# Kernel tuning notes

Hardware: AMD Instinct MI355X
Metric: run time of the kernel (lower is better)

The kernel has to match this reference:

```python
import jax, jax.numpy as jnp
import numpy as np

T, B, I, H, L, O = 512, 64, 128, 512, 2, 256


def _lstm_layer(x, Wih, Whh, b):
    """One LSTM layer over time. x:[T,B,in] -> (ys:[T,B,H], hT:[B,H], cT:[B,H]).
    PyTorch gate order: i, f, g, o. Zero initial state (module's zero buffers)."""
    Hs = Whh.shape[1]
    # Precompute input contribution for all timesteps (one big GEMM).
    xg = jnp.einsum('tbi,gi->tbg', x, Wih) + b  # [T,B,4H]

    def step(carry, xt):
        h, c = carry
        g = xt + h @ Whh.T  # [B,4H]
        i, f, gg, o = jnp.split(g, 4, axis=-1)
        c = jax.nn.sigmoid(f) * c + jax.nn.sigmoid(i) * jnp.tanh(gg)
        h = jax.nn.sigmoid(o) * jnp.tanh(c)
        return (h, c), h

    h0 = jnp.zeros((x.shape[1], Hs), x.dtype)
    (hT, cT), ys = jax.lax.scan(step, (h0, h0), xg)
    return ys, hT, cT


def setup_inputs() -> dict:
    key = jax.random.key(0)
    ks = jax.random.split(key, 9)
    s = 1.0 / np.sqrt(H)  # torch default uniform(-1/sqrt(H), 1/sqrt(H)) scale
    u = lambda k, shp: jax.random.uniform(k, shp, jnp.float32, -s, s)
    return {
        'x': jax.random.normal(ks[0], (T, B, I), jnp.float32),
        'W_ih0': u(ks[1], (4 * H, I)),
        'W_hh0': u(ks[2], (4 * H, H)),
        'b0': u(ks[3], (4 * H,)),  # b_ih + b_hh combined
        'W_ih1': u(ks[4], (4 * H, H)),
        'W_hh1': u(ks[5], (4 * H, H)),
        'b1': u(ks[6], (4 * H,)),
        'fc_w': u(ks[7], (O, H)),
        'fc_b': u(ks[8], (O,)),
    }


def reference(x, W_ih0, W_hh0, b0, W_ih1, W_hh1, b1, fc_w, fc_b):
    y0, h0, c0 = _lstm_layer(x, W_ih0, W_hh0, b0)
    y1, h1, c1 = _lstm_layer(y0, W_ih1, W_hh1, b1)
    fc = jnp.einsum('tbh,oh->tbo', y1, fc_w) + fc_b  # fused output projection
    hN = jnp.stack([h0, h1])  # [L,B,H]
    cN = jnp.stack([c0, c1])
    return fc, (hN, cN)
```

## Files before the change

kernel.cpp:

```cpp
#include <hip/hip_runtime.h>
#include <hip/hip_bf16.h>

#define T_SEQ 512
#define BATCH 64
#define IN0   128
#define HID   512
#define OUTF  256
#define G4    (4*HID)
#define NWG_L 64
#define FSTR  32

typedef __attribute__((ext_vector_type(8))) short short8;
typedef __attribute__((ext_vector_type(4))) float f32x4;
typedef unsigned short u16;
typedef unsigned long long u64;

__device__ __forceinline__ float sigmoidf_(float x) { return 1.f / (1.f + __expf(-x)); }
__device__ __forceinline__ float tanhf_(float x)    { return 1.f - 2.f / (1.f + __expf(2.f * x)); }

__device__ __forceinline__ u16 f2bf(float f) {
    union { float f; unsigned u; } a; a.f = f;
    unsigned u = a.u;
    return (u16)((u + 0x7fffu + ((u >> 16) & 1u)) >> 16);
}

__device__ __forceinline__ void poll_grp(const unsigned* flags, int lane, int grp, unsigned tgt) {
    const unsigned* p = flags + (size_t)(grp * 16 + (lane & 15)) * FSTR;
    unsigned it = 0;
    for (;;) {
        unsigned v = __hip_atomic_load(p, __ATOMIC_RELAXED, __HIP_MEMORY_SCOPE_AGENT);
        if (__all((int)(v >= tgt))) return;
        if (it < 6) __builtin_amdgcn_s_sleep(1);
        else        __builtin_amdgcn_s_sleep(16);
        if ((++it & 1023u) == 0u)
            (void)__hip_atomic_load(p, __ATOMIC_ACQUIRE, __HIP_MEMORY_SCOPE_AGENT);
    }
}

__global__ void cvt_f32_bf16(const float* __restrict__ in, u16* __restrict__ out, int n4) {
    int i = blockIdx.x * blockDim.x + threadIdx.x;
    if (i < n4) {
        float4 v = reinterpret_cast<const float4*>(in)[i];
        ushort4 o;
        o.x = f2bf(v.x); o.y = f2bf(v.y); o.z = f2bf(v.z); o.w = f2bf(v.w);
        reinterpret_cast<ushort4*>(out)[i] = o;
    }
}

template<int LAYER>
__device__ __forceinline__ void run_layer(
    const u16* __restrict__ asrc,
    const u16* __restrict__ wih, const u16* __restrict__ whh,
    const float* __restrict__ bias,
    u16* __restrict__ ybuf,
    float* __restrict__ hNout, float* __restrict__ cNout,
    unsigned* flags_own, unsigned* flags_dep, int g,
    u16 (*lds_w)[32][512], float (*lds_g)[33], float (*lds_b)[16],
    unsigned (*lds_h)[4])
{
    constexpr int KIN = (LAYER == 0) ? IN0 : HID;
    constexpr int KS1 = KIN / 32;
    constexpr int KS  = KS1 + 16;

    const int tid  = threadIdx.x;
    const int lane = tid & 63;
    const int w    = tid >> 6;
    const int ubase = 8 * g;

    for (int idx = tid; idx < 2 * KS * 64; idx += 256) {
        int nt  = (idx >= KS * 64) ? 1 : 0;
        int rem = idx - nt * KS * 64;
        int ks = rem >> 6, s = rem & 63, q = s & 15, kq = s >> 4;
        int r = (q >> 2) * HID + ubase + 4 * nt + (q & 3);
        const u16* src = (ks < KS1)
            ? wih + (size_t)r * KIN + (size_t)ks * 32 + kq * 8
            : whh + (size_t)r * HID + (size_t)(ks - KS1) * 32 + kq * 8;
        *reinterpret_cast<uint4*>(&lds_w[nt][ks][s * 8]) =
            *reinterpret_cast<const uint4*>(src);
    }
    if (tid < 32) {
        int nt = tid >> 4, q = tid & 15;
        lds_b[nt][q] = bias[(q >> 2) * HID + ubase + 4 * nt + (q & 3)];
    }
    __syncthreads();

    const int pb  = tid & 63;
    const int pu2 = tid >> 6;
    float c0 = 0.f, c1 = 0.f;

    const int arow = 16 * w + (lane & 15);
    const int koff = (lane >> 4) * 8;

    for (int t = 0; t < T_SEQ; ++t) {
        f32x4 ac0[4] = {{0,0,0,0},{0,0,0,0},{0,0,0,0},{0,0,0,0}};
        f32x4 ac1[4] = {{0,0,0,0},{0,0,0,0},{0,0,0,0},{0,0,0,0}};

        if (LAYER == 0) {
            const u16* ap = asrc + ((size_t)t * BATCH + arow) * KIN + koff;
            short8 a[KS1];
            #pragma unroll
            for (int j = 0; j < KS1; ++j)
                a[j] = *reinterpret_cast<const short8*>(ap + j * 32);
            #pragma unroll
            for (int j = 0; j < KS1; ++j) {
                ac0[j & 3] = __builtin_amdgcn_mfma_f32_16x16x32_bf16(
                    a[j], *reinterpret_cast<const short8*>(&lds_w[0][j][lane * 8]), ac0[j & 3], 0, 0, 0);
                ac1[j & 3] = __builtin_amdgcn_mfma_f32_16x16x32_bf16(
                    a[j], *reinterpret_cast<const short8*>(&lds_w[1][j][lane * 8]), ac1[j & 3], 0, 0, 0);
            }
        } else {
            const u16* ap = asrc + ((size_t)t * BATCH + arow) * HID + koff;
            for (int grp = 0; grp < 4; ++grp) {
                poll_grp(flags_dep, lane, grp, (unsigned)(t + 1));
                #pragma unroll
                for (int j = 0; j < 4; ++j) {
                    int ks = grp * 4 + j;
                    short8 a = *reinterpret_cast<const short8*>(ap + ks * 32);
                    ac0[j] = __builtin_amdgcn_mfma_f32_16x16x32_bf16(
                        a, *reinterpret_cast<const short8*>(&lds_w[0][ks][lane * 8]), ac0[j], 0, 0, 0);
                    ac1[j] = __builtin_amdgcn_mfma_f32_16x16x32_bf16(
                        a, *reinterpret_cast<const short8*>(&lds_w[1][ks][lane * 8]), ac1[j], 0, 0, 0);
                }
            }
        }

        if (t > 0) {
            const u16* hp = ybuf + ((size_t)(t - 1) * BATCH + arow) * HID + koff;
            for (int grp = 0; grp < 4; ++grp) {
                poll_grp(flags_own, lane, grp, (unsigned)t);
                #pragma unroll
                for (int j = 0; j < 4; ++j) {
                    int ks = grp * 4 + j;
                    short8 a = *reinterpret_cast<const short8*>(hp + ks * 32);
                    ac0[j] = __builtin_amdgcn_mfma_f32_16x16x32_bf16(
                        a, *reinterpret_cast<const short8*>(&lds_w[0][KS1 + ks][lane * 8]), ac0[j], 0, 0, 0);
                    ac1[j] = __builtin_amdgcn_mfma_f32_16x16x32_bf16(
                        a, *reinterpret_cast<const short8*>(&lds_w[1][KS1 + ks][lane * 8]), ac1[j], 0, 0, 0);
                }
            }
        }

        f32x4 s0 = (ac0[0] + ac0[1]) + (ac0[2] + ac0[3]);
        f32x4 s1 = (ac1[0] + ac1[1]) + (ac1[2] + ac1[3]);
        #pragma unroll
        for (int j = 0; j < 4; ++j) {
            int row = 16 * w + (lane >> 4) * 4 + j;
            lds_g[row][lane & 15]        = s0[j];
            lds_g[row][16 + (lane & 15)] = s1[j];
        }
        __syncthreads();

        {
            const int nt = pu2 >> 1;
            const int dq = (2 * pu2) & 3;
            const float* gr = &lds_g[pb][nt * 16];
            const float* br = lds_b[nt];
            float gi0 = sigmoidf_(gr[dq]      + br[dq]);
            float gf0 = sigmoidf_(gr[4 + dq]  + br[4 + dq]);
            float gg0 = tanhf_(   gr[8 + dq]  + br[8 + dq]);
            float go0 = sigmoidf_(gr[12 + dq] + br[12 + dq]);
            c0 = gf0 * c0 + gi0 * gg0;
            float h0v = go0 * tanhf_(c0);
            float gi1 = sigmoidf_(gr[dq + 1]      + br[dq + 1]);
            float gf1 = sigmoidf_(gr[4 + dq + 1]  + br[4 + dq + 1]);
            float gg1 = tanhf_(   gr[8 + dq + 1]  + br[8 + dq + 1]);
            float go1 = sigmoidf_(gr[12 + dq + 1] + br[12 + dq + 1]);
            c1 = gf1 * c1 + gi1 * gg1;
            float h1v = go1 * tanhf_(c1);

            lds_h[pb][pu2] = (unsigned)f2bf(h0v) | ((unsigned)f2bf(h1v) << 16);

            if (t == T_SEQ - 1) {
                const int u0 = ubase + 4 * nt + dq, u1 = u0 + 1;
                hNout[pb * HID + u0] = h0v;
                hNout[pb * HID + u1] = h1v;
                cNout[pb * HID + u0] = c0;
                cNout[pb * HID + u1] = c1;
            }
        }
        __syncthreads();

        if (w == 0) {
            uint4 hv = *reinterpret_cast<const uint4*>(&lds_h[lane][0]);
            u64 q0 = (u64)hv.x | ((u64)hv.y << 32);
            u64 q1 = (u64)hv.z | ((u64)hv.w << 32);
            u64* yp = reinterpret_cast<u64*>(
                ybuf + ((size_t)t * BATCH + lane) * HID + ubase);
            __hip_atomic_store(yp + 0, q0, __ATOMIC_RELAXED, __HIP_MEMORY_SCOPE_AGENT);
            __hip_atomic_store(yp + 1, q1, __ATOMIC_RELAXED, __HIP_MEMORY_SCOPE_AGENT);
            asm volatile("s_waitcnt vmcnt(0)" ::: "memory");
            if (lane == 0)
                __hip_atomic_store(flags_own + (size_t)g * FSTR, (unsigned)(t + 1),
                                   __ATOMIC_RELAXED, __HIP_MEMORY_SCOPE_AGENT);
        }
    }
}

__global__ __launch_bounds__(256, 1)
void lstm_fused(const u16* __restrict__ x_bf,
                const u16* __restrict__ wih0, const u16* __restrict__ whh0, const float* __restrict__ b0,
                const u16* __restrict__ wih1, const u16* __restrict__ whh1, const float* __restrict__ b1,
                u16* __restrict__ y0, u16* __restrict__ y1,
                float* __restrict__ hN, float* __restrict__ cN,
                unsigned* __restrict__ ctr)
{
    __shared__ __align__(16) u16 lds_w[2][32][512];
    __shared__ float lds_g[BATCH][33];
    __shared__ float lds_b[2][16];
    __shared__ __align__(16) unsigned lds_h[BATCH][4];

    unsigned* flags0 = ctr;
    unsigned* flags1 = ctr + NWG_L * FSTR;

    const int wgid = blockIdx.x;
    if (wgid < NWG_L) {
        run_layer<0>(x_bf, wih0, whh0, b0, y0, hN, cN,
                     flags0, flags0, wgid, lds_w, lds_g, lds_b, lds_h);
    } else {
        run_layer<1>(y0, wih1, whh1, b1, y1, hN + BATCH * HID, cN + BATCH * HID,
                     flags1, flags0, wgid - NWG_L, lds_w, lds_g, lds_b, lds_h);
    }
}

__global__ __launch_bounds__(256)
void fc_kernel(const u16* __restrict__ y1, const u16* __restrict__ fcw,
               const float* __restrict__ fcb, float* __restrict__ out)
{
    const int tid  = threadIdx.x;
    const int lane = tid & 63;
    const int wgid = blockIdx.x * 4 + (tid >> 6);
    const int nq   = wgid & 3;
    const int mt0  = wgid >> 2;

    for (int j = 0; j < 8; ++j) {
        int mt = mt0 + j * 256;
        f32x4 acc[4] = {{0,0,0,0},{0,0,0,0},{0,0,0,0},{0,0,0,0}};
        const u16* arow = y1 + ((size_t)mt * 16 + (lane & 15)) * HID + (lane >> 4) * 8;
        #pragma unroll
        for (int ks = 0; ks < 16; ++ks) {
            short8 a = *reinterpret_cast<const short8*>(arow + ks * 32);
            #pragma unroll
            for (int nt = 0; nt < 4; ++nt) {
                const u16* brow = fcw + ((size_t)(nq * 64 + nt * 16 + (lane & 15))) * HID
                                      + ks * 32 + (lane >> 4) * 8;
                short8 b = *reinterpret_cast<const short8*>(brow);
                acc[nt] = __builtin_amdgcn_mfma_f32_16x16x32_bf16(a, b, acc[nt], 0, 0, 0);
            }
        }
        #pragma unroll
        for (int nt = 0; nt < 4; ++nt) {
            int col = nq * 64 + nt * 16 + (lane & 15);
            float bb = fcb[col];
            #pragma unroll
            for (int jj = 0; jj < 4; ++jj) {
                int row = mt * 16 + (lane >> 4) * 4 + jj;
                out[(size_t)row * OUTF + col] = acc[nt][jj] + bb;
            }
        }
    }
}

extern "C" void kernel_launch(void* const* d_in, const int* in_sizes, int n_in,
                              void* d_out, int out_size, void* d_ws, size_t ws_size,
                              hipStream_t stream)
{
    const float* x    = (const float*)d_in[0];
    const float* wih0 = (const float*)d_in[1];
    const float* whh0 = (const float*)d_in[2];
    const float* b0   = (const float*)d_in[3];
    const float* wih1 = (const float*)d_in[4];
    const float* whh1 = (const float*)d_in[5];
    const float* b1   = (const float*)d_in[6];
    const float* fcw  = (const float*)d_in[7];
    const float* fcb  = (const float*)d_in[8];
    float* out = (float*)d_out;

    const size_t flag_bytes = (size_t)2 * NWG_L * FSTR * 4;

    char* ws = (char*)d_ws;
    size_t off = 0;
    unsigned* ctr = (unsigned*)ws;                    off += flag_bytes;
    u16* x_bf    = (u16*)(ws + off);                  off += (size_t)T_SEQ * BATCH * IN0 * 2;
    u16* wih0_bf = (u16*)(ws + off);                  off += (size_t)G4 * IN0 * 2;
    u16* whh0_bf = (u16*)(ws + off);                  off += (size_t)G4 * HID * 2;
    u16* wih1_bf = (u16*)(ws + off);                  off += (size_t)G4 * HID * 2;
    u16* whh1_bf = (u16*)(ws + off);                  off += (size_t)G4 * HID * 2;
    u16* fcw_bf  = (u16*)(ws + off);                  off += (size_t)OUTF * HID * 2;
    u16* y0      = (u16*)(ws + off);                  off += (size_t)T_SEQ * BATCH * HID * 2;
    u16* y1      = (u16*)(ws + off);                  off += (size_t)T_SEQ * BATCH * HID * 2;

    hipMemsetAsync(ctr, 0, flag_bytes, stream);

    auto conv = [&](const float* in, u16* o, int n) {
        int n4 = n / 4;
        cvt_f32_bf16<<<(n4 + 255) / 256, 256, 0, stream>>>(in, o, n4);
    };
    conv(x,    x_bf,    T_SEQ * BATCH * IN0);
    conv(wih0, wih0_bf, G4 * IN0);
    conv(whh0, whh0_bf, G4 * HID);
    conv(wih1, wih1_bf, G4 * HID);
    conv(whh1, whh1_bf, G4 * HID);
    conv(fcw,  fcw_bf,  OUTF * HID);

    float* outFC = out;
    float* hN = out + (size_t)T_SEQ * BATCH * OUTF;
    float* cN = hN + 2 * BATCH * HID;

    lstm_fused<<<2 * NWG_L, 256, 0, stream>>>(x_bf, wih0_bf, whh0_bf, b0,
                                              wih1_bf, whh1_bf, b1,
                                              y0, y1, hN, cN, ctr);
    fc_kernel<<<256, 256, 0, stream>>>(y1, fcw_bf, fcb, outFC);
}
```

Measured before the change: 3.302 ms.

## Halve LSTM workgroups per layer, each owning 16 hidden units

```diff
diff --git a/kernel.cpp b/kernel.cpp
--- a/kernel.cpp
+++ b/kernel.cpp
@@ -7,7 +7,7 @@
 #define HID   512
 #define OUTF  256
 #define G4    (4*HID)
-#define NWG_L 64
+#define NWG_L 32
 #define FSTR  32
 
 typedef __attribute__((ext_vector_type(8))) short short8;
@@ -25,7 +25,7 @@
 }
 
 __device__ __forceinline__ void poll_grp(const unsigned* flags, int lane, int grp, unsigned tgt) {
-    const unsigned* p = flags + (size_t)(grp * 16 + (lane & 15)) * FSTR;
+    const unsigned* p = flags + (size_t)(grp * 8 + (lane & 7)) * FSTR;
     unsigned it = 0;
     for (;;) {
         unsigned v = __hip_atomic_load(p, __ATOMIC_RELAXED, __HIP_MEMORY_SCOPE_AGENT);
@@ -55,8 +55,8 @@
     u16* __restrict__ ybuf,
     float* __restrict__ hNout, float* __restrict__ cNout,
     unsigned* flags_own, unsigned* flags_dep, int g,
-    u16 (*lds_w)[32][512], float (*lds_g)[33], float (*lds_b)[16],
-    unsigned (*lds_h)[4])
+    u16 (*lds_w)[32][512], float (*lds_g)[65], float (*lds_b)[16],
+    unsigned (*lds_h)[8])
 {
     constexpr int KIN = (LAYER == 0) ? IN0 : HID;
     constexpr int KS1 = KIN / 32;
@@ -65,11 +65,11 @@
     const int tid  = threadIdx.x;
     const int lane = tid & 63;
     const int w    = tid >> 6;
-    const int ubase = 8 * g;
-
-    for (int idx = tid; idx < 2 * KS * 64; idx += 256) {
-        int nt  = (idx >= KS * 64) ? 1 : 0;
-        int rem = idx - nt * KS * 64;
+    const int ubase = 16 * g;
+
+    for (int idx = tid; idx < 4 * KS * 64; idx += 256) {
+        int nt  = idx / (KS * 64);
+        int rem = idx - nt * (KS * 64);
         int ks = rem >> 6, s = rem & 63, q = s & 15, kq = s >> 4;
         int r = (q >> 2) * HID + ubase + 4 * nt + (q & 3);
         const u16* src = (ks < KS1)
@@ -78,22 +78,21 @@
         *reinterpret_cast<uint4*>(&lds_w[nt][ks][s * 8]) =
             *reinterpret_cast<const uint4*>(src);
     }
-    if (tid < 32) {
+    if (tid < 64) {
         int nt = tid >> 4, q = tid & 15;
         lds_b[nt][q] = bias[(q >> 2) * HID + ubase + 4 * nt + (q & 3)];
     }
     __syncthreads();
 
-    const int pb  = tid & 63;
-    const int pu2 = tid >> 6;
-    float c0 = 0.f, c1 = 0.f;
+    const int pb = tid & 63;
+    const int pw = tid >> 6;
+    float cst[4] = {0.f, 0.f, 0.f, 0.f};
 
     const int arow = 16 * w + (lane & 15);
     const int koff = (lane >> 4) * 8;
 
     for (int t = 0; t < T_SEQ; ++t) {
-        f32x4 ac0[4] = {{0,0,0,0},{0,0,0,0},{0,0,0,0},{0,0,0,0}};
-        f32x4 ac1[4] = {{0,0,0,0},{0,0,0,0},{0,0,0,0},{0,0,0,0}};
+        f32x4 ac[4] = {{0,0,0,0},{0,0,0,0},{0,0,0,0},{0,0,0,0}};
 
         if (LAYER == 0) {
             const u16* ap = asrc + ((size_t)t * BATCH + arow) * KIN + koff;
@@ -102,12 +101,11 @@
             for (int j = 0; j < KS1; ++j)
                 a[j] = *reinterpret_cast<const short8*>(ap + j * 32);
             #pragma unroll
-            for (int j = 0; j < KS1; ++j) {
-                ac0[j & 3] = __builtin_amdgcn_mfma_f32_16x16x32_bf16(
-                    a[j], *reinterpret_cast<const short8*>(&lds_w[0][j][lane * 8]), ac0[j & 3], 0, 0, 0);
-                ac1[j & 3] = __builtin_amdgcn_mfma_f32_16x16x32_bf16(
-                    a[j], *reinterpret_cast<const short8*>(&lds_w[1][j][lane * 8]), ac1[j & 3], 0, 0, 0);
-            }
+            for (int j = 0; j < KS1; ++j)
+                #pragma unroll
+                for (int nt = 0; nt < 4; ++nt)
+                    ac[nt] = __builtin_amdgcn_mfma_f32_16x16x32_bf16(
+                        a[j], *reinterpret_cast<const short8*>(&lds_w[nt][j][lane * 8]), ac[nt], 0, 0, 0);
         } else {
             const u16* ap = asrc + ((size_t)t * BATCH + arow) * HID + koff;
             for (int grp = 0; grp < 4; ++grp) {
@@ -116,10 +114,10 @@
                 for (int j = 0; j < 4; ++j) {
                     int ks = grp * 4 + j;
                     short8 a = *reinterpret_cast<const short8*>(ap + ks * 32);
-                    ac0[j] = __builtin_amdgcn_mfma_f32_16x16x32_bf16(
-                        a, *reinterpret_cast<const short8*>(&lds_w[0][ks][lane * 8]), ac0[j], 0, 0, 0);
-                    ac1[j] = __builtin_amdgcn_mfma_f32_16x16x32_bf16(
-                        a, *reinterpret_cast<const short8*>(&lds_w[1][ks][lane * 8]), ac1[j], 0, 0, 0);
+                    #pragma unroll
+                    for (int nt = 0; nt < 4; ++nt)
+                        ac[nt] = __builtin_amdgcn_mfma_f32_16x16x32_bf16(
+                            a, *reinterpret_cast<const short8*>(&lds_w[nt][ks][lane * 8]), ac[nt], 0, 0, 0);
                 }
             }
         }
@@ -132,62 +130,60 @@
                 for (int j = 0; j < 4; ++j) {
                     int ks = grp * 4 + j;
                     short8 a = *reinterpret_cast<const short8*>(hp + ks * 32);
-                    ac0[j] = __builtin_amdgcn_mfma_f32_16x16x32_bf16(
-                        a, *reinterpret_cast<const short8*>(&lds_w[0][KS1 + ks][lane * 8]), ac0[j], 0, 0, 0);
-                    ac1[j] = __builtin_amdgcn_mfma_f32_16x16x32_bf16(
-                        a, *reinterpret_cast<const short8*>(&lds_w[1][KS1 + ks][lane * 8]), ac1[j], 0, 0, 0);
+                    #pragma unroll
+                    for (int nt = 0; nt < 4; ++nt)
+                        ac[nt] = __builtin_amdgcn_mfma_f32_16x16x32_bf16(
+                            a, *reinterpret_cast<const short8*>(&lds_w[nt][KS1 + ks][lane * 8]), ac[nt], 0, 0, 0);
                 }
             }
         }
 
-        f32x4 s0 = (ac0[0] + ac0[1]) + (ac0[2] + ac0[3]);
-        f32x4 s1 = (ac1[0] + ac1[1]) + (ac1[2] + ac1[3]);
         #pragma unroll
         for (int j = 0; j < 4; ++j) {
             int row = 16 * w + (lane >> 4) * 4 + j;
-            lds_g[row][lane & 15]        = s0[j];
-            lds_g[row][16 + (lane & 15)] = s1[j];
+            #pragma unroll
+            for (int nt = 0; nt < 4; ++nt)
+                lds_g[row][nt * 16 + (lane & 15)] = ac[nt][j];
         }
         __syncthreads();
 
         {
-            const int nt = pu2 >> 1;
-            const int dq = (2 * pu2) & 3;
-            const float* gr = &lds_g[pb][nt * 16];
-            const float* br = lds_b[nt];
-            float gi0 = sigmoidf_(gr[dq]      + br[dq]);
-            float gf0 = sigmoidf_(gr[4 + dq]  + br[4 + dq]);
-            float gg0 = tanhf_(   gr[8 + dq]  + br[8 + dq]);
-            float go0 = sigmoidf_(gr[12 + dq] + br[12 + dq]);
-            c0 = gf0 * c0 + gi0 * gg0;
-            float h0v = go0 * tanhf_(c0);
-            float gi1 = sigmoidf_(gr[dq + 1]      + br[dq + 1]);
-            float gf1 = sigmoidf_(gr[4 + dq + 1]  + br[4 + dq + 1]);
-            float gg1 = tanhf_(   gr[8 + dq + 1]  + br[8 + dq + 1]);
-            float go1 = sigmoidf_(gr[12 + dq + 1] + br[12 + dq + 1]);
-            c1 = gf1 * c1 + gi1 * gg1;
-            float h1v = go1 * tanhf_(c1);
-
-            lds_h[pb][pu2] = (unsigned)f2bf(h0v) | ((unsigned)f2bf(h1v) << 16);
-
-            if (t == T_SEQ - 1) {
-                const int u0 = ubase + 4 * nt + dq, u1 = u0 + 1;
-                hNout[pb * HID + u0] = h0v;
-                hNout[pb * HID + u1] = h1v;
-                cNout[pb * HID + u0] = c0;
-                cNout[pb * HID + u1] = c1;
-            }
+            const float* gr = &lds_g[pb][pw * 16];
+            const float* br = lds_b[pw];
+            unsigned hv[4];
+            #pragma unroll
+            for (int k = 0; k < 4; ++k) {
+                float gi = sigmoidf_(gr[k]      + br[k]);
+                float gf = sigmoidf_(gr[4 + k]  + br[4 + k]);
+                float gg = tanhf_(   gr[8 + k]  + br[8 + k]);
+                float go = sigmoidf_(gr[12 + k] + br[12 + k]);
+                cst[k] = gf * cst[k] + gi * gg;
+                float h = go * tanhf_(cst[k]);
+                hv[k] = (unsigned)f2bf(h);
+                if (t == T_SEQ - 1) {
+                    const int u = ubase + 4 * pw + k;
+                    hNout[pb * HID + u] = h;
+                    cNout[pb * HID + u] = cst[k];
+                }
+            }
+            lds_h[pb][2 * pw]     = hv[0] | (hv[1] << 16);
+            lds_h[pb][2 * pw + 1] = hv[2] | (hv[3] << 16);
         }
         __syncthreads();
 
         if (w == 0) {
-            uint4 hv = *reinterpret_cast<const uint4*>(&lds_h[lane][0]);
-            u64 q0 = (u64)hv.x | ((u64)hv.y << 32);
-            u64 q1 = (u64)hv.z | ((u64)hv.w << 32);
+            uint4 h0 = *reinterpret_cast<const uint4*>(&lds_h[lane][0]);
+            uint4 h1 = *reinterpret_cast<const uint4*>(&lds_h[lane][4]);
+            u64 q0 = (u64)h0.x | ((u64)h0.y << 32);
+            u64 q1 = (u64)h0.z | ((u64)h0.w << 32);
+            u64 q2 = (u64)h1.x | ((u64)h1.y << 32);
+            u64 q3 = (u64)h1.z | ((u64)h1.w << 32);
             u64* yp = reinterpret_cast<u64*>(
                 ybuf + ((size_t)t * BATCH + lane) * HID + ubase);
             __hip_atomic_store(yp + 0, q0, __ATOMIC_RELAXED, __HIP_MEMORY_SCOPE_AGENT);
             __hip_atomic_store(yp + 1, q1, __ATOMIC_RELAXED, __HIP_MEMORY_SCOPE_AGENT);
+            __hip_atomic_store(yp + 2, q2, __ATOMIC_RELAXED, __HIP_MEMORY_SCOPE_AGENT);
+            __hip_atomic_store(yp + 3, q3, __ATOMIC_RELAXED, __HIP_MEMORY_SCOPE_AGENT);
             asm volatile("s_waitcnt vmcnt(0)" ::: "memory");
             if (lane == 0)
                 __hip_atomic_store(flags_own + (size_t)g * FSTR, (unsigned)(t + 1),
@@ -204,10 +200,10 @@
                 float* __restrict__ hN, float* __restrict__ cN,
                 unsigned* __restrict__ ctr)
 {
-    __shared__ __align__(16) u16 lds_w[2][32][512];
-    __shared__ float lds_g[BATCH][33];
-    __shared__ float lds_b[2][16];
-    __shared__ __align__(16) unsigned lds_h[BATCH][4];
+    __shared__ __align__(16) u16 lds_w[4][32][512];
+    __shared__ float lds_g[BATCH][65];
+    __shared__ float lds_b[4][16];
+    __shared__ __align__(16) unsigned lds_h[BATCH][8];
 
     unsigned* flags0 = ctr;
     unsigned* flags1 = ctr + NWG_L * FSTR;
```

Result: slower. 4.032 ms (+22.1%).

## Poll all dependency flags at once and batch all activation loads before MFMAs

Applied to the files above, without the earlier changes.

```diff
diff --git a/kernel.cpp b/kernel.cpp
--- a/kernel.cpp
+++ b/kernel.cpp
@@ -24,16 +24,23 @@
     return (u16)((u + 0x7fffu + ((u >> 16) & 1u)) >> 16);
 }
 
-__device__ __forceinline__ void poll_grp(const unsigned* flags, int lane, int grp, unsigned tgt) {
-    const unsigned* p = flags + (size_t)(grp * 16 + (lane & 15)) * FSTR;
+template<int LAYER>
+__device__ __forceinline__ void poll_all(const unsigned* fo, const unsigned* fd,
+                                         int lane, unsigned to, unsigned td) {
+    const unsigned* po = fo + (size_t)lane * FSTR;
+    const unsigned* pd = fd + (size_t)lane * FSTR;
     unsigned it = 0;
     for (;;) {
-        unsigned v = __hip_atomic_load(p, __ATOMIC_RELAXED, __HIP_MEMORY_SCOPE_AGENT);
-        if (__all((int)(v >= tgt))) return;
+        bool ok = true;
+        if (to)
+            ok = __hip_atomic_load(po, __ATOMIC_RELAXED, __HIP_MEMORY_SCOPE_AGENT) >= to;
+        if (LAYER == 1)
+            ok = ok && (__hip_atomic_load(pd, __ATOMIC_RELAXED, __HIP_MEMORY_SCOPE_AGENT) >= td);
+        if (__all((int)ok)) return;
         if (it < 6) __builtin_amdgcn_s_sleep(1);
         else        __builtin_amdgcn_s_sleep(16);
         if ((++it & 1023u) == 0u)
-            (void)__hip_atomic_load(p, __ATOMIC_ACQUIRE, __HIP_MEMORY_SCOPE_AGENT);
+            (void)__hip_atomic_load(po, __ATOMIC_ACQUIRE, __HIP_MEMORY_SCOPE_AGENT);
     }
 }
 
@@ -108,35 +115,55 @@
                 ac1[j & 3] = __builtin_amdgcn_mfma_f32_16x16x32_bf16(
                     a[j], *reinterpret_cast<const short8*>(&lds_w[1][j][lane * 8]), ac1[j & 3], 0, 0, 0);
             }
-        } else {
+        }
+
+        if (LAYER == 1 || t > 0)
+            poll_all<LAYER>(flags_own, flags_dep, lane, (unsigned)t, (unsigned)(t + 1));
+
+        if (LAYER == 1) {
             const u16* ap = asrc + ((size_t)t * BATCH + arow) * HID + koff;
-            for (int grp = 0; grp < 4; ++grp) {
-                poll_grp(flags_dep, lane, grp, (unsigned)(t + 1));
+            short8 ay[16];
+            #pragma unroll
+            for (int j = 0; j < 16; ++j)
+                ay[j] = *reinterpret_cast<const short8*>(ap + j * 32);
+            if (t > 0) {
+                const u16* hp = ybuf + ((size_t)(t - 1) * BATCH + arow) * HID + koff;
+                short8 ah[16];
                 #pragma unroll
-                for (int j = 0; j < 4; ++j) {
-                    int ks = grp * 4 + j;
-                    short8 a = *reinterpret_cast<const short8*>(ap + ks * 32);
-                    ac0[j] = __builtin_amdgcn_mfma_f32_16x16x32_bf16(
-                        a, *reinterpret_cast<const short8*>(&lds_w[0][ks][lane * 8]), ac0[j], 0, 0, 0);
-                    ac1[j] = __builtin_amdgcn_mfma_f32_16x16x32_bf16(
-                        a, *reinterpret_cast<const short8*>(&lds_w[1][ks][lane * 8]), ac1[j], 0, 0, 0);
+                for (int j = 0; j < 16; ++j)
+                    ah[j] = *reinterpret_cast<const short8*>(hp + j * 32);
+                #pragma unroll
+                for (int j = 0; j < 16; ++j) {
+                    ac0[j & 3] = __builtin_amdgcn_mfma_f32_16x16x32_bf16(
+                        ay[j], *reinterpret_cast<const short8*>(&lds_w[0][j][lane * 8]), ac0[j & 3], 0, 0, 0);
+                    ac1[j & 3] = __builtin_amdgcn_mfma_f32_16x16x32_bf16(
+                        ay[j], *reinterpret_cast<const short8*>(&lds_w[1][j][lane * 8]), ac1[j & 3], 0, 0, 0);
+                    ac0[j & 3] = __builtin_amdgcn_mfma_f32_16x16x32_bf16(
+                        ah[j], *reinterpret_cast<const short8*>(&lds_w[0][KS1 + j][lane * 8]), ac0[j & 3], 0, 0, 0);
+                    ac1[j & 3] = __builtin_amdgcn_mfma_f32_16x16x32_bf16(
+                        ah[j], *reinterpret_cast<const short8*>(&lds_w[1][KS1 + j][lane * 8]), ac1[j & 3], 0, 0, 0);
                 }
-            }
-        }
-
-        if (t > 0) {
+            } else {
+                #pragma unroll
+                for (int j = 0; j < 16; ++j) {
+                    ac0[j & 3] = __builtin_amdgcn_mfma_f32_16x16x32_bf16(
+                        ay[j], *reinterpret_cast<const short8*>(&lds_w[0][j][lane * 8]), ac0[j & 3], 0, 0, 0);
+                    ac1[j & 3] = __builtin_amdgcn_mfma_f32_16x16x32_bf16(
+                        ay[j], *reinterpret_cast<const short8*>(&lds_w[1][j][lane * 8]), ac1[j & 3], 0, 0, 0);
+                }
+            }
+        } else if (t > 0) {
             const u16* hp = ybuf + ((size_t)(t - 1) * BATCH + arow) * HID + koff;
-            for (int grp = 0; grp < 4; ++grp) {
-                poll_grp(flags_own, lane, grp, (unsigned)t);
-                #pragma unroll
-                for (int j = 0; j < 4; ++j) {
-                    int ks = grp * 4 + j;
-                    short8 a = *reinterpret_cast<const short8*>(hp + ks * 32);
-                    ac0[j] = __builtin_amdgcn_mfma_f32_16x16x32_bf16(
-                        a, *reinterpret_cast<const short8*>(&lds_w[0][KS1 + ks][lane * 8]), ac0[j], 0, 0, 0);
-                    ac1[j] = __builtin_amdgcn_mfma_f32_16x16x32_bf16(
-                        a, *reinterpret_cast<const short8*>(&lds_w[1][KS1 + ks][lane * 8]), ac1[j], 0, 0, 0);
-                }
+            short8 ah[16];
+            #pragma unroll
+            for (int j = 0; j < 16; ++j)
+                ah[j] = *reinterpret_cast<const short8*>(hp + j * 32);
+            #pragma unroll
+            for (int j = 0; j < 16; ++j) {
+                ac0[j & 3] = __builtin_amdgcn_mfma_f32_16x16x32_bf16(
+                    ah[j], *reinterpret_cast<const short8*>(&lds_w[0][KS1 + j][lane * 8]), ac0[j & 3], 0, 0, 0);
+                ac1[j & 3] = __builtin_amdgcn_mfma_f32_16x16x32_bf16(
+                    ah[j], *reinterpret_cast<const short8*>(&lds_w[1][KS1 + j][lane * 8]), ac1[j & 3], 0, 0, 0);
             }
         }
 
@@ -180,7 +207,7 @@
         }
         __syncthreads();
 
-        if (w == 0) {
+        if (w == (t & 3)) {
             uint4 hv = *reinterpret_cast<const uint4*>(&lds_h[lane][0]);
             u64 q0 = (u64)hv.x | ((u64)hv.y << 32);
             u64 q1 = (u64)hv.z | ((u64)hv.w << 32);
```

Result: slower. 3.651 ms (+10.6%).

## Tag hidden-state words with timestep and validate data on load

Applied to the files above, without the earlier changes.

```diff
diff --git a/kernel.cpp b/kernel.cpp
--- a/kernel.cpp
+++ b/kernel.cpp
@@ -9,6 +9,7 @@
 #define G4    (4*HID)
 #define NWG_L 64
 #define FSTR  32
+#define RING  8
 
 typedef __attribute__((ext_vector_type(8))) short short8;
 typedef __attribute__((ext_vector_type(4))) float f32x4;
@@ -37,6 +38,45 @@
     }
 }
 
+__device__ __forceinline__ void load_grp_tagged(
+    const unsigned* rp, unsigned tagv, int grp, short8 (&a)[4])
+{
+    uint4 lo[4], hi[4];
+    #pragma unroll
+    for (int j = 0; j < 4; ++j) {
+        const uint4* q = reinterpret_cast<const uint4*>(rp + (grp * 4 + j) * 32);
+        lo[j] = q[0]; hi[j] = q[1];
+    }
+    for (;;) {
+        unsigned bad = 0;
+        #pragma unroll
+        for (int j = 0; j < 4; ++j) {
+            bool ok = (lo[j].x >> 16) == tagv && (lo[j].y >> 16) == tagv
+                   && (lo[j].z >> 16) == tagv && (lo[j].w >> 16) == tagv
+                   && (hi[j].x >> 16) == tagv && (hi[j].y >> 16) == tagv
+                   && (hi[j].z >> 16) == tagv && (hi[j].w >> 16) == tagv;
+            if (!ok) bad |= 1u << j;
+        }
+        if (__all((int)(bad == 0))) break;
+        __builtin_amdgcn_s_sleep(1);
+        #pragma unroll
+        for (int j = 0; j < 4; ++j) if (bad & (1u << j)) {
+            const unsigned* q = rp + (grp * 4 + j) * 32;
+            asm volatile("global_load_dwordx4 %0, %2, off sc1\n\t"
+                         "global_load_dwordx4 %1, %2, off offset:16 sc1"
+                         : "=v"(lo[j]), "=v"(hi[j]) : "v"(q));
+        }
+        asm volatile("s_waitcnt vmcnt(0)" ::: "memory");
+    }
+    #pragma unroll
+    for (int j = 0; j < 4; ++j) {
+        a[j][0] = (short)lo[j].x; a[j][1] = (short)lo[j].y;
+        a[j][2] = (short)lo[j].z; a[j][3] = (short)lo[j].w;
+        a[j][4] = (short)hi[j].x; a[j][5] = (short)hi[j].y;
+        a[j][6] = (short)hi[j].z; a[j][7] = (short)hi[j].w;
+    }
+}
+
 __global__ void cvt_f32_bf16(const float* __restrict__ in, u16* __restrict__ out, int n4) {
     int i = blockIdx.x * blockDim.x + threadIdx.x;
     if (i < n4) {
@@ -49,14 +89,17 @@
 
 template<int LAYER>
 __device__ __forceinline__ void run_layer(
-    const u16* __restrict__ asrc,
-    const u16* __restrict__ wih, const u16* __restrict__ whh,
+    const u16* __restrict__ x_bf,
+    const unsigned* __restrict__ dep_tag,
+    unsigned* __restrict__ own_tag,
+    u16* __restrict__ y1bf,
+    const float* __restrict__ wih, const float* ,
+    const u16* __restrict__ wihb, const u16* __restrict__ whhb,
     const float* __restrict__ bias,
-    u16* __restrict__ ybuf,
     float* __restrict__ hNout, float* __restrict__ cNout,
     unsigned* flags_own, unsigned* flags_dep, int g,
     u16 (*lds_w)[32][512], float (*lds_g)[33], float (*lds_b)[16],
-    unsigned (*lds_h)[4])
+    unsigned (*lds_h)[8])
 {
     constexpr int KIN = (LAYER == 0) ? IN0 : HID;
     constexpr int KS1 = KIN / 32;
@@ -73,8 +116,8 @@
         int ks = rem >> 6, s = rem & 63, q = s & 15, kq = s >> 4;
         int r = (q >> 2) * HID + ubase + 4 * nt + (q & 3);
         const u16* src = (ks < KS1)
-            ? wih + (size_t)r * KIN + (size_t)ks * 32 + kq * 8
-            : whh + (size_t)r * HID + (size_t)(ks - KS1) * 32 + kq * 8;
+            ? wihb + (size_t)r * KIN + (size_t)ks * 32 + kq * 8
+            : whhb + (size_t)r * HID + (size_t)(ks - KS1) * 32 + kq * 8;
         *reinterpret_cast<uint4*>(&lds_w[nt][ks][s * 8]) =
             *reinterpret_cast<const uint4*>(src);
     }
@@ -92,11 +135,12 @@
     const int koff = (lane >> 4) * 8;
 
     for (int t = 0; t < T_SEQ; ++t) {
+        const unsigned tagv = (unsigned)(t + 1);
         f32x4 ac0[4] = {{0,0,0,0},{0,0,0,0},{0,0,0,0},{0,0,0,0}};
         f32x4 ac1[4] = {{0,0,0,0},{0,0,0,0},{0,0,0,0},{0,0,0,0}};
 
         if (LAYER == 0) {
-            const u16* ap = asrc + ((size_t)t * BATCH + arow) * KIN + koff;
+            const u16* ap = x_bf + ((size_t)t * BATCH + arow) * KIN + koff;
             short8 a[KS1];
             #pragma unroll
             for (int j = 0; j < KS1; ++j)
@@ -109,33 +153,36 @@
                     a[j], *reinterpret_cast<const short8*>(&lds_w[1][j][lane * 8]), ac1[j & 3], 0, 0, 0);
             }
         } else {
-            const u16* ap = asrc + ((size_t)t * BATCH + arow) * HID + koff;
+            const unsigned* rp = dep_tag + ((size_t)t * BATCH + arow) * HID + koff;
             for (int grp = 0; grp < 4; ++grp) {
-                poll_grp(flags_dep, lane, grp, (unsigned)(t + 1));
+                poll_grp(flags_dep, lane, grp, tagv);
+                short8 a[4];
+                load_grp_tagged(rp, tagv, grp, a);
                 #pragma unroll
                 for (int j = 0; j < 4; ++j) {
                     int ks = grp * 4 + j;
-                    short8 a = *reinterpret_cast<const short8*>(ap + ks * 32);
                     ac0[j] = __builtin_amdgcn_mfma_f32_16x16x32_bf16(
-                        a, *reinterpret_cast<const short8*>(&lds_w[0][ks][lane * 8]), ac0[j], 0, 0, 0);
+                        a[j], *reinterpret_cast<const short8*>(&lds_w[0][ks][lane * 8]), ac0[j], 0, 0, 0);
                     ac1[j] = __builtin_amdgcn_mfma_f32_16x16x32_bf16(
-                        a, *reinterpret_cast<const short8*>(&lds_w[1][ks][lane * 8]), ac1[j], 0, 0, 0);
+                        a[j], *reinterpret_cast<const short8*>(&lds_w[1][ks][lane * 8]), ac1[j], 0, 0, 0);
                 }
             }
         }
 
         if (t > 0) {
-            const u16* hp = ybuf + ((size_t)(t - 1) * BATCH + arow) * HID + koff;
+            const size_t slot = (LAYER == 0) ? (size_t)(t - 1) : (size_t)((t - 1) & (RING - 1));
+            const unsigned* rp = own_tag + (slot * BATCH + arow) * HID + koff;
             for (int grp = 0; grp < 4; ++grp) {
                 poll_grp(flags_own, lane, grp, (unsigned)t);
+                short8 a[4];
+                load_grp_tagged(rp, (unsigned)t, grp, a);
                 #pragma unroll
                 for (int j = 0; j < 4; ++j) {
                     int ks = grp * 4 + j;
-                    short8 a = *reinterpret_cast<const short8*>(hp + ks * 32);
                     ac0[j] = __builtin_amdgcn_mfma_f32_16x16x32_bf16(
-                        a, *reinterpret_cast<const short8*>(&lds_w[0][KS1 + ks][lane * 8]), ac0[j], 0, 0, 0);
+                        a[j], *reinterpret_cast<const short8*>(&lds_w[0][KS1 + ks][lane * 8]), ac0[j], 0, 0, 0);
                     ac1[j] = __builtin_amdgcn_mfma_f32_16x16x32_bf16(
-                        a, *reinterpret_cast<const short8*>(&lds_w[1][KS1 + ks][lane * 8]), ac1[j], 0, 0, 0);
+                        a[j], *reinterpret_cast<const short8*>(&lds_w[1][KS1 + ks][lane * 8]), ac1[j], 0, 0, 0);
                 }
             }
         }
@@ -168,7 +215,8 @@
             c1 = gf1 * c1 + gi1 * gg1;
             float h1v = go1 * tanhf_(c1);
 
-            lds_h[pb][pu2] = (unsigned)f2bf(h0v) | ((unsigned)f2bf(h1v) << 16);
+            lds_h[pb][4 * nt + dq]     = (unsigned)f2bf(h0v) | (tagv << 16);
+            lds_h[pb][4 * nt + dq + 1] = (unsigned)f2bf(h1v) | (tagv << 16);
 
             if (t == T_SEQ - 1) {
                 const int u0 = ubase + 4 * nt + dq, u1 = u0 + 1;
@@ -181,43 +229,61 @@
         __syncthreads();
 
         if (w == 0) {
-            uint4 hv = *reinterpret_cast<const uint4*>(&lds_h[lane][0]);
-            u64 q0 = (u64)hv.x | ((u64)hv.y << 32);
-            u64 q1 = (u64)hv.z | ((u64)hv.w << 32);
-            u64* yp = reinterpret_cast<u64*>(
-                ybuf + ((size_t)t * BATCH + lane) * HID + ubase);
-            __hip_atomic_store(yp + 0, q0, __ATOMIC_RELAXED, __HIP_MEMORY_SCOPE_AGENT);
-            __hip_atomic_store(yp + 1, q1, __ATOMIC_RELAXED, __HIP_MEMORY_SCOPE_AGENT);
-            asm volatile("s_waitcnt vmcnt(0)" ::: "memory");
+            const unsigned* hr = lds_h[lane];
+            u64 q0 = (u64)hr[0] | ((u64)hr[1] << 32);
+            u64 q1 = (u64)hr[2] | ((u64)hr[3] << 32);
+            u64 q2 = (u64)hr[4] | ((u64)hr[5] << 32);
+            u64 q3 = (u64)hr[6] | ((u64)hr[7] << 32);
+            const size_t slot = (LAYER == 0) ? (size_t)t : (size_t)(t & (RING - 1));
+            u64* hp = reinterpret_cast<u64*>(
+                own_tag + (slot * BATCH + lane) * HID + ubase);
+            __hip_atomic_store(hp + 0, q0, __ATOMIC_RELAXED, __HIP_MEMORY_SCOPE_AGENT);
+            __hip_atomic_store(hp + 1, q1, __ATOMIC_RELAXED, __HIP_MEMORY_SCOPE_AGENT);
+            __hip_atomic_store(hp + 2, q2, __ATOMIC_RELAXED, __HIP_MEMORY_SCOPE_AGENT);
+            __hip_atomic_store(hp + 3, q3, __ATOMIC_RELAXED, __HIP_MEMORY_SCOPE_AGENT);
+            if (LAYER == 1) {
+                uint4 pk;
+                pk.x = (hr[0] & 0xffffu) | (hr[1] << 16);
+                pk.y = (hr[2] & 0xffffu) | (hr[3] << 16);
+                pk.z = (hr[4] & 0xffffu) | (hr[5] << 16);
+                pk.w = (hr[6] & 0xffffu) | (hr[7] << 16);
+                *reinterpret_cast<uint4*>(
+                    y1bf + ((size_t)t * BATCH + lane) * HID + ubase) = pk;
+            }
             if (lane == 0)
-                __hip_atomic_store(flags_own + (size_t)g * FSTR, (unsigned)(t + 1),
+                __hip_atomic_store(flags_own + (size_t)g * FSTR, tagv,
                                    __ATOMIC_RELAXED, __HIP_MEMORY_SCOPE_AGENT);
         }
     }
+    asm volatile("s_waitcnt vmcnt(0)" ::: "memory");
 }
 
 __global__ __launch_bounds__(256, 1)
 void lstm_fused(const u16* __restrict__ x_bf,
-                const u16* __restrict__ wih0, const u16* __restrict__ whh0, const float* __restrict__ b0,
-                const u16* __restrict__ wih1, const u16* __restrict__ whh1, const float* __restrict__ b1,
-                u16* __restrict__ y0, u16* __restrict__ y1,
+                const u16* __restrict__ wih0b, const u16* __restrict__ whh0b, const float* __restrict__ b0,
+                const u16* __restrict__ wih1b, const u16* __restrict__ whh1b, const float* __restrict__ b1,
+                unsigned* __restrict__ y0tag, unsigned* __restrict__ ring1,
+                u16* __restrict__ y1bf,
                 float* __restrict__ hN, float* __restrict__ cN,
                 unsigned* __restrict__ ctr)
 {
     __shared__ __align__(16) u16 lds_w[2][32][512];
     __shared__ float lds_g[BATCH][33];
     __shared__ float lds_b[2][16];
-    __shared__ __align__(16) unsigned lds_h[BATCH][4];
+    __shared__ __align__(16) unsigned lds_h[BATCH][8];
 
     unsigned* flags0 = ctr;
     unsigned* flags1 = ctr + NWG_L * FSTR;
 
     const int wgid = blockIdx.x;
     if (wgid < NWG_L) {
-        run_layer<0>(x_bf, wih0, whh0, b0, y0, hN, cN,
+        run_layer<0>(x_bf, nullptr, y0tag, nullptr,
+                     nullptr, nullptr, wih0b, whh0b, b0, hN, cN,
                      flags0, flags0, wgid, lds_w, lds_g, lds_b, lds_h);
     } else {
-        run_layer<1>(y0, wih1, whh1, b1, y1, hN + BATCH * HID, cN + BATCH * HID,
+        run_layer<1>(nullptr, y0tag, ring1, y1bf,
+                     nullptr, nullptr, wih1b, whh1b, b1,
+                     hN + BATCH * HID, cN + BATCH * HID,
                      flags1, flags0, wgid - NWG_L, lds_w, lds_g, lds_b, lds_h);
     }
 }
@@ -286,8 +352,9 @@
     u16* wih1_bf = (u16*)(ws + off);                  off += (size_t)G4 * HID * 2;
     u16* whh1_bf = (u16*)(ws + off);                  off += (size_t)G4 * HID * 2;
     u16* fcw_bf  = (u16*)(ws + off);                  off += (size_t)OUTF * HID * 2;
-    u16* y0      = (u16*)(ws + off);                  off += (size_t)T_SEQ * BATCH * HID * 2;
-    u16* y1      = (u16*)(ws + off);                  off += (size_t)T_SEQ * BATCH * HID * 2;
+    unsigned* y0tag = (unsigned*)(ws + off);          off += (size_t)T_SEQ * BATCH * HID * 4;
+    unsigned* ring1 = (unsigned*)(ws + off);          off += (size_t)RING * BATCH * HID * 4;
+    u16* y1bf    = (u16*)(ws + off);                  off += (size_t)T_SEQ * BATCH * HID * 2;
 
     hipMemsetAsync(ctr, 0, flag_bytes, stream);
 
@@ -308,6 +375,6 @@
 
     lstm_fused<<<2 * NWG_L, 256, 0, stream>>>(x_bf, wih0_bf, whh0_bf, b0,
                                               wih1_bf, whh1_bf, b1,
-                                              y0, y1, hN, cN, ctr);
-    fc_kernel<<<256, 256, 0, stream>>>(y1, fcw_bf, fcb, outFC);
-}
+                                              y0tag, ring1, y1bf, hN, cN, ctr);
+    fc_kernel<<<256, 256, 0, stream>>>(y1bf, fcw_bf, fcb, outFC);
+}
```

New measurement: 6.200 ms. 1.88x slower.
